# Kernel optimization log

Hardware: AMD Instinct MI355X
Metric: run time of the kernel (lower is better)

Reference implementation:

```python
import jax, jax.numpy as jnp
import numpy as np

NUM_CLASSES = 20
LAMBDA_COORD = 5.0
BATCH_SIZE = 512
ANCHORS = [[1.3221, 1.73145], [3.19275, 4.00944], [5.05587, 8.09892],
           [9.47112, 4.84053], [11.2364, 10.0071]]


def setup_inputs() -> dict:
    key = jax.random.key(0)
    k1, k2 = jax.random.split(key)
    prediction = jax.random.normal(k1, (512, 125, 13, 13), dtype=jnp.float32)
    # target: conf in [0,1), xy in [0,1), wh positive -> uniform is a valid fill
    target = jax.random.uniform(k2, (512, 13, 13, 125), dtype=jnp.float32)
    anchors = jnp.asarray(ANCHORS, dtype=jnp.float32)
    return {"prediction": prediction, "target": target, "anchors": anchors}


def _pairwise_iou(a, b):
    """a, b: [B, HW, A, 4] center-format (x, y, w, h).
    Returns pairwise IoU [B, HW, A, A] between a-anchors and b-boxes."""
    a = a[..., :, None, :]  # [B,HW,A,1,4]
    b = b[..., None, :, :]  # [B,HW,1,A,4]
    ax1, ay1 = a[..., 0] - a[..., 2] * 0.5, a[..., 1] - a[..., 3] * 0.5
    ax2, ay2 = a[..., 0] + a[..., 2] * 0.5, a[..., 1] + a[..., 3] * 0.5
    bx1, by1 = b[..., 0] - b[..., 2] * 0.5, b[..., 1] - b[..., 3] * 0.5
    bx2, by2 = b[..., 0] + b[..., 2] * 0.5, b[..., 1] + b[..., 3] * 0.5
    iw = jnp.clip(jnp.minimum(ax2, bx2) - jnp.maximum(ax1, bx1), 0.0)
    ih = jnp.clip(jnp.minimum(ay2, by2) - jnp.maximum(ay1, by1), 0.0)
    inter = iw * ih
    area_a = (ax2 - ax1) * (ay2 - ay1)
    area_b = (bx2 - bx1) * (by2 - by1)
    return inter / (area_a + area_b - inter + 1e-10)


def reference(prediction, target, anchors):
    bsize, _, h, w = prediction.shape
    A = anchors.shape[0]
    C = 5 + NUM_CLASSES
    out = jnp.transpose(prediction, (0, 2, 3, 1)).reshape(bsize, h * w * A, C)
    tgt = target.reshape(bsize, h * w * A, C)

    # decode predictions
    pred_xy = jax.nn.sigmoid(out[..., 21:23])
    pred_wh = jnp.exp(out[..., 23:25])
    pred_box = jnp.concatenate([pred_xy, pred_wh], axis=-1).reshape(bsize, h * w, A, 4)

    gt_box = jnp.concatenate([tgt[..., 21:23], tgt[..., 23:25]], axis=-1)
    gt_box = gt_box.reshape(bsize, h * w, A, 4)
    gt_conf = tgt[..., 20].reshape(bsize, h * w, A, 1)

    # anchor boxes: predicted centers with prior (anchor) width/height
    anc_wh = jnp.broadcast_to(anchors[None, None], (bsize, h * w, A, 2))
    anc_box = jnp.concatenate([pred_box[..., :2], anc_wh], axis=-1)

    iou = _pairwise_iou(anc_box, gt_box)            # [B, HW, A, A]
    anchor_idx = jnp.argmax(iou, axis=-1)           # [B, HW, A]

    # torch fancy-index write mask[:, :, anchor_idx, :] = gt_conf[:, :, anchor_idx, :]
    # assigns gt_conf at every anchor slot whose index appears anywhere in anchor_idx;
    # uncovered slots stay zero.
    covered = jnp.zeros((A,), dtype=bool).at[anchor_idx.reshape(-1)].set(True)
    mask = jnp.where(covered[None, None, :, None], gt_conf, 0.0)

    diff = pred_box * mask - gt_box * mask
    box_loss = (LAMBDA_COORD / BATCH_SIZE) * jnp.sum(diff * diff)
    return box_loss
```

## Files before the change

kernel.cpp:

```cpp
#include <hip/hip_runtime.h>
#include <math.h>

#define NB 512
#define HW 169
#define NA 5
#define NCH 125
#define BLOCK 256
#define NBLOCKS ((NB * HW) / BLOCK)
#define REC 8

__global__ __launch_bounds__(BLOCK, 1) void yolo_loss_main(
    const float* __restrict__ P,
    const float* __restrict__ T,
    const float* __restrict__ ANC,
    float* __restrict__ brec)
{
    int t = threadIdx.x;
    int idx = blockIdx.x * BLOCK + t;
    int b  = idx / HW;
    int hw = idx - b * HW;

    const float* Pb = P + (size_t)b * NCH * HW + hw;
    const float* Tb = T + ((size_t)b * HW + hw) * NCH;

    float gx[NA], gy[NA], gw_[NA], gh[NA], gc[NA];
    float rx[NA], ry[NA], rw[NA], rh[NA];
#pragma unroll
    for (int a = 0; a < NA; ++a) {
        int c0 = a * 25;
        gc[a]  = Tb[c0 + 20];
        gx[a]  = Tb[c0 + 21];
        gy[a]  = Tb[c0 + 22];
        gw_[a] = Tb[c0 + 23];
        gh[a]  = Tb[c0 + 24];
    }
#pragma unroll
    for (int a = 0; a < NA; ++a) {
        int c0 = a * 25;
        rx[a] = Pb[(c0 + 21) * HW];
        ry[a] = Pb[(c0 + 22) * HW];
        rw[a] = Pb[(c0 + 23) * HW];
        rh[a] = Pb[(c0 + 24) * HW];
    }
    __builtin_amdgcn_sched_barrier(0);

    float px[NA], py[NA], pw[NA], ph[NA];
#pragma unroll
    for (int a = 0; a < NA; ++a) {
        px[a] = 1.0f / (1.0f + expf(-rx[a]));
        py[a] = 1.0f / (1.0f + expf(-ry[a]));
        pw[a] = expf(rw[a]);
        ph[a] = expf(rh[a]);
    }

    float contrib[NA];
    int cmask = 0;
#pragma unroll
    for (int i = 0; i < NA; ++i) {
        float aw = ANC[2 * i], ah = ANC[2 * i + 1];
        float ax1 = px[i] - aw * 0.5f, ax2 = px[i] + aw * 0.5f;
        float ay1 = py[i] - ah * 0.5f, ay2 = py[i] + ah * 0.5f;
        float area_a = (ax2 - ax1) * (ay2 - ay1);
        float best = -1.0f; int bestj = 0;
#pragma unroll
        for (int j = 0; j < NA; ++j) {
            float bx1 = gx[j] - gw_[j] * 0.5f, bx2 = gx[j] + gw_[j] * 0.5f;
            float by1 = gy[j] - gh[j] * 0.5f, by2 = gy[j] + gh[j] * 0.5f;
            float iw = fmaxf(fminf(ax2, bx2) - fmaxf(ax1, bx1), 0.0f);
            float ih = fmaxf(fminf(ay2, by2) - fmaxf(ay1, by1), 0.0f);
            float inter = iw * ih;
            float area_b = (bx2 - bx1) * (by2 - by1);
            float iou = inter / (area_a + area_b - inter + 1e-10f);
            if (iou > best) { best = iou; bestj = j; }
        }
        cmask |= (1 << bestj);
        float dx = px[i] - gx[i], dy = py[i] - gy[i];
        float dw = pw[i] - gw_[i], dh = ph[i] - gh[i];
        contrib[i] = gc[i] * gc[i] * (dx * dx + dy * dy + dw * dw + dh * dh);
    }

    __shared__ float sred[4][NA];
    __shared__ int smask[4];
    int lane = t & 63, wid = t >> 6;

#pragma unroll
    for (int i = 0; i < NA; ++i) {
        float v = contrib[i];
        for (int off = 32; off; off >>= 1) v += __shfl_down(v, off, 64);
        if (lane == 0) sred[wid][i] = v;
    }
    for (int off = 32; off; off >>= 1) cmask |= __shfl_down(cmask, off, 64);
    if (lane == 0) smask[wid] = cmask;
    __syncthreads();

    if (t == 0) {
        int m = smask[0] | smask[1] | smask[2] | smask[3];
        float* r = brec + blockIdx.x * REC;
#pragma unroll
        for (int i = 0; i < NA; ++i)
            r[i] = sred[0][i] + sred[1][i] + sred[2][i] + sred[3][i];
        ((int*)r)[5] = m;
        ((int*)r)[6] = 0;
        ((int*)r)[7] = 0;
    }
}

__global__ void yolo_loss_final(const float* __restrict__ brec,
                                float* __restrict__ out)
{
    int lane = threadIdx.x;
    const float4* r4 = (const float4*)brec;
    double s[NA] = {0, 0, 0, 0, 0};
    int m = 0;
    for (int e = lane; e < NBLOCKS; e += 64) {
        float4 lo = r4[e * 2];
        float4 hi = r4[e * 2 + 1];
        s[0] += (double)lo.x; s[1] += (double)lo.y;
        s[2] += (double)lo.z; s[3] += (double)lo.w;
        s[4] += (double)hi.x;
        m |= __float_as_int(hi.y);
    }
#pragma unroll
    for (int i = 0; i < NA; ++i)
        for (int off = 32; off; off >>= 1) s[i] += __shfl_down(s[i], off, 64);
    for (int off = 32; off; off >>= 1) m |= __shfl_down(m, off, 64);

    if (lane == 0) {
        double tot = 0.0;
#pragma unroll
        for (int i = 0; i < NA; ++i)
            if ((m >> i) & 1) tot += s[i];
        out[0] = (float)((5.0 / 512.0) * tot);
    }
}

extern "C" void kernel_launch(void* const* d_in, const int* in_sizes, int n_in,
                              void* d_out, int out_size, void* d_ws, size_t ws_size,
                              hipStream_t stream) {
    const float* P   = (const float*)d_in[0];
    const float* T   = (const float*)d_in[1];
    const float* ANC = (const float*)d_in[2];
    float* out = (float*)d_out;

    float* brec = (float*)d_ws;

    yolo_loss_main<<<NBLOCKS, BLOCK, 0, stream>>>(P, T, ANC, brec);
    yolo_loss_final<<<1, 64, 0, stream>>>(brec, out);
}
```

Measured before the change: 20.86 us.

## Fuse final reduction into main kernel via last-block atomic counter

Drops the separate single-block finalize kernel. Each block now writes its partial sums with atomic stores and bumps a global counter, and the last block to arrive does the final reduction and writes the output. A memset that resets the counter is added to the stream each call, replacing the second kernel launch. It also changes launch bounds to allow two blocks per CU and removes the scheduling barrier. The memset launch and the serialized tail inside the last block may offset the saved launch gap.

```diff
diff --git a/kernel.cpp b/kernel.cpp
--- a/kernel.cpp
+++ b/kernel.cpp
@@ -9,11 +9,16 @@
 #define NBLOCKS ((NB * HW) / BLOCK)
 #define REC 8
 
-__global__ __launch_bounds__(BLOCK, 1) void yolo_loss_main(
+__device__ __forceinline__ float u2f_(unsigned int u) { return __uint_as_float(u); }
+__device__ __forceinline__ unsigned int f2u_(float f) { return __float_as_uint(f); }
+
+__global__ __launch_bounds__(BLOCK, 2) void yolo_loss_fused(
     const float* __restrict__ P,
     const float* __restrict__ T,
     const float* __restrict__ ANC,
-    float* __restrict__ brec)
+    unsigned int* __restrict__ wsrec,
+    unsigned int* __restrict__ counter,
+    float* __restrict__ out)
 {
     int t = threadIdx.x;
     int idx = blockIdx.x * BLOCK + t;
@@ -42,7 +47,6 @@
         rw[a] = Pb[(c0 + 23) * HW];
         rh[a] = Pb[(c0 + 24) * HW];
     }
-    __builtin_amdgcn_sched_barrier(0);
 
     float px[NA], py[NA], pw[NA], ph[NA];
 #pragma unroll
@@ -81,6 +85,7 @@
 
     __shared__ float sred[4][NA];
     __shared__ int smask[4];
+    __shared__ int swin;
     int lane = t & 63, wid = t >> 6;
 
 #pragma unroll
@@ -95,42 +100,47 @@
 
     if (t == 0) {
         int m = smask[0] | smask[1] | smask[2] | smask[3];
-        float* r = brec + blockIdx.x * REC;
+        unsigned int* r = wsrec + blockIdx.x * REC;
+#pragma unroll
+        for (int i = 0; i < NA; ++i) {
+            float s = sred[0][i] + sred[1][i] + sred[2][i] + sred[3][i];
+            __hip_atomic_store(&r[i], f2u_(s), __ATOMIC_RELAXED, __HIP_MEMORY_SCOPE_AGENT);
+        }
+        __hip_atomic_store(&r[5], (unsigned int)m, __ATOMIC_RELAXED, __HIP_MEMORY_SCOPE_AGENT);
+        unsigned int old = __hip_atomic_fetch_add(counter, 1u, __ATOMIC_ACQ_REL,
+                                                  __HIP_MEMORY_SCOPE_AGENT);
+        swin = (old == NBLOCKS - 1);
+    }
+    __syncthreads();
+
+    if (swin && t < 64) {
+        double s[NA] = {0, 0, 0, 0, 0};
+        int m = 0;
+        for (int e = t; e < NBLOCKS; e += 64) {
+            const unsigned int* r = wsrec + e * REC;
+            unsigned int w0 = __hip_atomic_load(&r[0], __ATOMIC_RELAXED, __HIP_MEMORY_SCOPE_AGENT);
+            unsigned int w1 = __hip_atomic_load(&r[1], __ATOMIC_RELAXED, __HIP_MEMORY_SCOPE_AGENT);
+            unsigned int w2 = __hip_atomic_load(&r[2], __ATOMIC_RELAXED, __HIP_MEMORY_SCOPE_AGENT);
+            unsigned int w3 = __hip_atomic_load(&r[3], __ATOMIC_RELAXED, __HIP_MEMORY_SCOPE_AGENT);
+            unsigned int w4 = __hip_atomic_load(&r[4], __ATOMIC_RELAXED, __HIP_MEMORY_SCOPE_AGENT);
+            unsigned int w5 = __hip_atomic_load(&r[5], __ATOMIC_RELAXED, __HIP_MEMORY_SCOPE_AGENT);
+            s[0] += (double)u2f_(w0); s[1] += (double)u2f_(w1);
+            s[2] += (double)u2f_(w2); s[3] += (double)u2f_(w3);
+            s[4] += (double)u2f_(w4);
+            m |= (int)w5;
+        }
 #pragma unroll
         for (int i = 0; i < NA; ++i)
-            r[i] = sred[0][i] + sred[1][i] + sred[2][i] + sred[3][i];
-        ((int*)r)[5] = m;
-        ((int*)r)[6] = 0;
-        ((int*)r)[7] = 0;
-    }
-}
+            for (int off = 32; off; off >>= 1) s[i] += __shfl_down(s[i], off, 64);
+        for (int off = 32; off; off >>= 1) m |= __shfl_down(m, off, 64);
 
-__global__ void yolo_loss_final(const float* __restrict__ brec,
-                                float* __restrict__ out)
-{
-    int lane = threadIdx.x;
-    const float4* r4 = (const float4*)brec;
-    double s[NA] = {0, 0, 0, 0, 0};
-    int m = 0;
-    for (int e = lane; e < NBLOCKS; e += 64) {
-        float4 lo = r4[e * 2];
-        float4 hi = r4[e * 2 + 1];
-        s[0] += (double)lo.x; s[1] += (double)lo.y;
-        s[2] += (double)lo.z; s[3] += (double)lo.w;
-        s[4] += (double)hi.x;
-        m |= __float_as_int(hi.y);
-    }
+        if (t == 0) {
+            double tot = 0.0;
 #pragma unroll
-    for (int i = 0; i < NA; ++i)
-        for (int off = 32; off; off >>= 1) s[i] += __shfl_down(s[i], off, 64);
-    for (int off = 32; off; off >>= 1) m |= __shfl_down(m, off, 64);
-
-    if (lane == 0) {
-        double tot = 0.0;
-#pragma unroll
-        for (int i = 0; i < NA; ++i)
-            if ((m >> i) & 1) tot += s[i];
-        out[0] = (float)((5.0 / 512.0) * tot);
+            for (int i = 0; i < NA; ++i)
+                if ((m >> i) & 1) tot += s[i];
+            out[0] = (float)((5.0 / 512.0) * tot);
+        }
     }
 }
 
@@ -142,8 +152,9 @@
     const float* ANC = (const float*)d_in[2];
     float* out = (float*)d_out;
 
-    float* brec = (float*)d_ws;
+    unsigned int* wsrec  = (unsigned int*)d_ws;
+    unsigned int* counter = wsrec + NBLOCKS * REC;
 
-    yolo_loss_main<<<NBLOCKS, BLOCK, 0, stream>>>(P, T, ANC, brec);
-    yolo_loss_final<<<1, 64, 0, stream>>>(brec, out);
+    hipMemsetAsync(counter, 0, sizeof(unsigned int), stream);
+    yolo_loss_fused<<<NBLOCKS, BLOCK, 0, stream>>>(P, T, ANC, wsrec, counter, out);
 }
```

Result: slower. 27.13 us (+30.1%).

## Coalesce target loads via shared-memory staging with 64-thread blocks

Applied to the files above, without the earlier changes.

Target channels 20-24 for a block of 64 cells are now loaded cooperatively with lane-contiguous indexing, staged through shared memory, then redistributed per thread. This replaces the strided per-thread loads that hit 125-float-separated addresses. Block size drops to one wavefront, so the cross-wave shared reduction goes away and each block writes its record with two float4 stores. The final reducer widens to 256 threads to handle the four-fold larger number of block records. The trade-off is more blocks, more partial records and a shared-memory round trip.

```diff
diff --git a/kernel.cpp b/kernel.cpp
--- a/kernel.cpp
+++ b/kernel.cpp
@@ -5,35 +5,37 @@
 #define HW 169
 #define NA 5
 #define NCH 125
-#define BLOCK 256
+#define BLOCK 64
 #define NBLOCKS ((NB * HW) / BLOCK)
 #define REC 8
 
-__global__ __launch_bounds__(BLOCK, 1) void yolo_loss_main(
+__global__ __launch_bounds__(BLOCK, 2) void yolo_loss_main(
     const float* __restrict__ P,
     const float* __restrict__ T,
     const float* __restrict__ ANC,
     float* __restrict__ brec)
 {
+    __shared__ float sT[BLOCK * 25];
+
     int t = threadIdx.x;
-    int idx = blockIdx.x * BLOCK + t;
+    int cell0 = blockIdx.x * BLOCK;
+
+    float tv[25];
+#pragma unroll
+    for (int r = 0; r < 25; ++r) {
+        int n  = r * 64 + t;
+        int cl = n / 25;
+        int s  = n - cl * 25;
+        int a  = s / 5;
+        int k  = s - a * 5;
+        tv[r] = T[(size_t)(cell0 + cl) * NCH + a * 25 + 20 + k];
+    }
+
+    int idx = cell0 + t;
     int b  = idx / HW;
     int hw = idx - b * HW;
-
     const float* Pb = P + (size_t)b * NCH * HW + hw;
-    const float* Tb = T + ((size_t)b * HW + hw) * NCH;
-
-    float gx[NA], gy[NA], gw_[NA], gh[NA], gc[NA];
     float rx[NA], ry[NA], rw[NA], rh[NA];
-#pragma unroll
-    for (int a = 0; a < NA; ++a) {
-        int c0 = a * 25;
-        gc[a]  = Tb[c0 + 20];
-        gx[a]  = Tb[c0 + 21];
-        gy[a]  = Tb[c0 + 22];
-        gw_[a] = Tb[c0 + 23];
-        gh[a]  = Tb[c0 + 24];
-    }
 #pragma unroll
     for (int a = 0; a < NA; ++a) {
         int c0 = a * 25;
@@ -42,7 +44,21 @@
         rw[a] = Pb[(c0 + 23) * HW];
         rh[a] = Pb[(c0 + 24) * HW];
     }
-    __builtin_amdgcn_sched_barrier(0);
+
+#pragma unroll
+    for (int r = 0; r < 25; ++r)
+        sT[r * 64 + t] = tv[r];
+    __syncthreads();
+
+    float gx[NA], gy[NA], gw_[NA], gh[NA], gc[NA];
+#pragma unroll
+    for (int a = 0; a < NA; ++a) {
+        gc[a]  = sT[t * 25 + a * 5 + 0];
+        gx[a]  = sT[t * 25 + a * 5 + 1];
+        gy[a]  = sT[t * 25 + a * 5 + 2];
+        gw_[a] = sT[t * 25 + a * 5 + 3];
+        gh[a]  = sT[t * 25 + a * 5 + 4];
+    }
 
     float px[NA], py[NA], pw[NA], ph[NA];
 #pragma unroll
@@ -79,40 +95,29 @@
         contrib[i] = gc[i] * gc[i] * (dx * dx + dy * dy + dw * dw + dh * dh);
     }
 
-    __shared__ float sred[4][NA];
-    __shared__ int smask[4];
-    int lane = t & 63, wid = t >> 6;
-
 #pragma unroll
-    for (int i = 0; i < NA; ++i) {
-        float v = contrib[i];
-        for (int off = 32; off; off >>= 1) v += __shfl_down(v, off, 64);
-        if (lane == 0) sred[wid][i] = v;
-    }
+    for (int i = 0; i < NA; ++i)
+        for (int off = 32; off; off >>= 1) contrib[i] += __shfl_down(contrib[i], off, 64);
     for (int off = 32; off; off >>= 1) cmask |= __shfl_down(cmask, off, 64);
-    if (lane == 0) smask[wid] = cmask;
-    __syncthreads();
 
     if (t == 0) {
-        int m = smask[0] | smask[1] | smask[2] | smask[3];
-        float* r = brec + blockIdx.x * REC;
-#pragma unroll
-        for (int i = 0; i < NA; ++i)
-            r[i] = sred[0][i] + sred[1][i] + sred[2][i] + sred[3][i];
-        ((int*)r)[5] = m;
-        ((int*)r)[6] = 0;
-        ((int*)r)[7] = 0;
+        float4* r4 = (float4*)(brec + blockIdx.x * REC);
+        r4[0] = make_float4(contrib[0], contrib[1], contrib[2], contrib[3]);
+        r4[1] = make_float4(contrib[4], __int_as_float(cmask), 0.0f, 0.0f);
     }
 }
 
-__global__ void yolo_loss_final(const float* __restrict__ brec,
-                                float* __restrict__ out)
+__global__ __launch_bounds__(256) void yolo_loss_final(
+    const float* __restrict__ brec, float* __restrict__ out)
 {
-    int lane = threadIdx.x;
+    __shared__ double sred[4][NA];
+    __shared__ int smask[4];
+    int t = threadIdx.x, lane = t & 63, wid = t >> 6;
     const float4* r4 = (const float4*)brec;
+
     double s[NA] = {0, 0, 0, 0, 0};
     int m = 0;
-    for (int e = lane; e < NBLOCKS; e += 64) {
+    for (int e = t; e < NBLOCKS; e += 256) {
         float4 lo = r4[e * 2];
         float4 hi = r4[e * 2 + 1];
         s[0] += (double)lo.x; s[1] += (double)lo.y;
@@ -124,12 +129,20 @@
     for (int i = 0; i < NA; ++i)
         for (int off = 32; off; off >>= 1) s[i] += __shfl_down(s[i], off, 64);
     for (int off = 32; off; off >>= 1) m |= __shfl_down(m, off, 64);
+    if (lane == 0) {
+#pragma unroll
+        for (int i = 0; i < NA; ++i) sred[wid][i] = s[i];
+        smask[wid] = m;
+    }
+    __syncthreads();
 
-    if (lane == 0) {
+    if (t == 0) {
+        int mm = smask[0] | smask[1] | smask[2] | smask[3];
         double tot = 0.0;
 #pragma unroll
         for (int i = 0; i < NA; ++i)
-            if ((m >> i) & 1) tot += s[i];
+            if ((mm >> i) & 1)
+                tot += sred[0][i] + sred[1][i] + sred[2][i] + sred[3][i];
         out[0] = (float)((5.0 / 512.0) * tot);
     }
 }
@@ -145,5 +158,5 @@
     float* brec = (float*)d_ws;
 
     yolo_loss_main<<<NBLOCKS, BLOCK, 0, stream>>>(P, T, ANC, brec);
-    yolo_loss_final<<<1, 64, 0, stream>>>(brec, out);
+    yolo_loss_final<<<1, 256, 0, stream>>>(brec, out);
 }
```

Result: slower. 21.67 us (+3.9%).
